# Performance work log

Hardware: AMD Instinct MI355X
Metric: run time of the kernel (lower is better)

## Reference

```python
import jax, jax.numpy as jnp
import numpy as np

D_EMBED = 768
N_HEAD = 12
D_ATTN = D_EMBED // N_HEAD  # 64
SCALE = 1.0 / np.sqrt(D_ATTN)


def setup_inputs() -> dict:
    key = jax.random.key(0)
    ks = jax.random.split(key, 5)
    B, S = 1, 4096
    x = jax.random.normal(ks[0], (B, S, D_EMBED), dtype=jnp.float32)
    # Linear weights stored as [in, out]; init std 0.02 as in _init_weights
    Wq = jax.random.normal(ks[1], (D_EMBED, D_EMBED), dtype=jnp.float32) * 0.02
    Wk = jax.random.normal(ks[2], (D_EMBED, D_EMBED), dtype=jnp.float32) * 0.02
    Wv = jax.random.normal(ks[3], (D_EMBED, D_EMBED), dtype=jnp.float32) * 0.02
    Wo = jax.random.normal(ks[4], (D_EMBED, D_EMBED), dtype=jnp.float32) * 0.02
    gamma = jnp.ones((N_HEAD,), dtype=jnp.float32)
    return {"x": x, "Wq": Wq, "Wk": Wk, "Wv": Wv, "Wo": Wo, "gamma": gamma}


def reference(x, Wq, Wk, Wv, Wo, gamma):
    B, S, _ = x.shape
    # QKV projections (self-attention: k = v = q = x)
    def split_heads(y):
        return y.reshape(B, S, N_HEAD, D_ATTN).transpose(0, 2, 1, 3)  # [B,H,S,D]
    q = split_heads(x @ Wq)
    k = split_heads(x @ Wk)
    v = split_heads(x @ Wv)
    # RBF attention scores: exp(-gamma * scale * ||q - k||^2)
    q_norm = jnp.sum(q * q, axis=-1, keepdims=True)            # [B,H,S,1]
    k_norm = jnp.sum(k * k, axis=-1, keepdims=True)            # [B,H,S,1]
    qk = jnp.einsum('bhsd,bhtd->bhst', q, k)                   # [B,H,S,S]
    dist = jnp.maximum(q_norm - 2.0 * qk + jnp.swapaxes(k_norm, -2, -1), 0.0)
    g = gamma.reshape(1, N_HEAD, 1, 1)
    scores = jnp.exp(-g * SCALE * dist)                        # [B,H,S,S]
    # attn @ V, merge heads, output proj (dropout p=0 -> identity)
    out = jnp.einsum('bhst,bhtd->bhsd', scores, v)
    out = out.transpose(0, 2, 1, 3).reshape(B, S, D_EMBED)
    return out @ Wo
```

## Files before the change

kernel.cpp:

```cpp
#include <hip/hip_runtime.h>
#include <stdint.h>


typedef __attribute__((ext_vector_type(4))) float f32x4;
typedef __attribute__((ext_vector_type(8))) short s16x8;
typedef __attribute__((ext_vector_type(2))) unsigned int u32x2;
typedef __attribute__((ext_vector_type(4))) unsigned int u32x4;

#define S_LEN 4096
#define NHEAD 12
#define DE 768

__device__ __forceinline__ uint16_t f2bf(float f) {
  unsigned u = __float_as_uint(f);
  u += 0x7fffu + ((u >> 16) & 1u);
  return (uint16_t)(u >> 16);
}

__device__ __forceinline__ void gll16(const void* g, void* l) {
  __builtin_amdgcn_global_load_lds(
      (const __attribute__((address_space(1))) unsigned int*)g,
      (__attribute__((address_space(3))) unsigned int*)l, 16, 0, 0);
}

__global__ void k_cvt_x(const float* __restrict__ x, uint16_t* __restrict__ xb) {
  int i = (blockIdx.x * 256 + threadIdx.x) * 4;
  float4 v = *(const float4*)(x + i);
  u32x2 o;
  o.x = (unsigned)f2bf(v.x) | ((unsigned)f2bf(v.y) << 16);
  o.y = (unsigned)f2bf(v.z) | ((unsigned)f2bf(v.w) << 16);
  *(u32x2*)(xb + i) = o;
}

__global__ void k_cvt_w(const float* __restrict__ W0, const float* __restrict__ W1,
                        const float* __restrict__ W2, const float* __restrict__ W3,
                        uint16_t* __restrict__ T0, uint16_t* __restrict__ T1,
                        uint16_t* __restrict__ T2, uint16_t* __restrict__ T3) {
  __shared__ float tile[64][65];
  int z = blockIdx.z;
  const float* W = z == 0 ? W0 : z == 1 ? W1 : z == 2 ? W2 : W3;
  uint16_t* T = z == 0 ? T0 : z == 1 ? T1 : z == 2 ? T2 : T3;
  int r0 = blockIdx.y * 64, c0 = blockIdx.x * 64;
  int t = threadIdx.x;
#pragma unroll
  for (int ii = 0; ii < 16; ++ii) {
    int idx = ii * 256 + t;
    int r = idx >> 6, c = idx & 63;
    tile[r][c] = W[(r0 + r) * DE + c0 + c];
  }
  __syncthreads();
#pragma unroll
  for (int ii = 0; ii < 16; ++ii) {
    int idx = ii * 256 + t;
    int r = idx >> 6, c = idx & 63;
    T[(size_t)(c0 + r) * DE + (r0 + c)] = f2bf(tile[c][r]);
  }
}

template <int MODE>
__global__ __launch_bounds__(256) void k_gemm(
    const uint16_t* __restrict__ A, const uint16_t* __restrict__ B0,
    const uint16_t* __restrict__ B1, const uint16_t* __restrict__ B2,
    uint16_t* __restrict__ Oq, uint16_t* __restrict__ Ok, uint16_t* __restrict__ Ov,
    float* __restrict__ OF) {
  __shared__ __align__(16) uint16_t As[128 * 64];
  __shared__ __align__(16) uint16_t Bs[128 * 64];
  const int K = DE;
  int z = (MODE == 0) ? blockIdx.z : 0;
  const uint16_t* Bt = (MODE == 0) ? (z == 0 ? B0 : z == 1 ? B1 : B2) : B0;
  int m0 = blockIdx.x * 128, n0 = blockIdx.y * 128;
  int tid = threadIdx.x, lane = tid & 63, wid = tid >> 6;
  int G = lane >> 4, c = lane & 15;
  int wr = (wid >> 1) * 64, wc = (wid & 1) * 64;
  f32x4 acc[4][4] = {};
  const char* AsB = (const char*)As;
  const char* BsB = (const char*)Bs;
  for (int kt = 0; kt < K / 64; ++kt) {
#pragma unroll
    for (int i = 0; i < 4; ++i) {
      int L = (i * 256 + tid) * 16;
      int row = L >> 7, ch = (L >> 4) & 7;
      int gch = ch ^ (row & 7);
      gll16((const char*)A + ((size_t)(m0 + row) * K + kt * 64) * 2 + gch * 16,
            (char*)As + i * 4096 + wid * 1024);
      gll16((const char*)Bt + ((size_t)(n0 + row) * K + kt * 64) * 2 + gch * 16,
            (char*)Bs + i * 4096 + wid * 1024);
    }
    __syncthreads();
#pragma unroll
    for (int ks = 0; ks < 2; ++ks) {
      s16x8 a[4], b[4];
#pragma unroll
      for (int mi = 0; mi < 4; ++mi) {
        int row = wr + mi * 16 + c;
        a[mi] = *(const s16x8*)(AsB + row * 128 + (((G + 4 * ks) ^ (row & 7)) << 4));
      }
#pragma unroll
      for (int ni = 0; ni < 4; ++ni) {
        int row = wc + ni * 16 + c;
        b[ni] = *(const s16x8*)(BsB + row * 128 + (((G + 4 * ks) ^ (row & 7)) << 4));
      }
#pragma unroll
      for (int mi = 0; mi < 4; ++mi)
#pragma unroll
        for (int ni = 0; ni < 4; ++ni)
          acc[mi][ni] = __builtin_amdgcn_mfma_f32_16x16x32_bf16(a[mi], b[ni], acc[mi][ni], 0, 0, 0);
    }
    __syncthreads();
  }
#pragma unroll
  for (int mi = 0; mi < 4; ++mi) {
#pragma unroll
    for (int ni = 0; ni < 4; ++ni) {
      int r = m0 + wr + mi * 16 + G * 4;
      int n = n0 + wc + ni * 16 + c;
      if (MODE == 0) {
        int h = n >> 6, d = n & 63;
        if (z < 2) {
          uint16_t* O = (z == 0) ? Oq : Ok;
#pragma unroll
          for (int rr = 0; rr < 4; ++rr)
            O[((size_t)h * S_LEN + (r + rr)) * 64 + d] = f2bf(acc[mi][ni][rr]);
        } else {
          u32x2 pk;
          pk.x = (unsigned)f2bf(acc[mi][ni][0]) | ((unsigned)f2bf(acc[mi][ni][1]) << 16);
          pk.y = (unsigned)f2bf(acc[mi][ni][2]) | ((unsigned)f2bf(acc[mi][ni][3]) << 16);
          *(u32x2*)(Ov + ((size_t)(h * 64 + d)) * S_LEN + r) = pk;
        }
      } else {
#pragma unroll
        for (int rr = 0; rr < 4; ++rr) OF[(size_t)(r + rr) * DE + n] = acc[mi][ni][rr];
      }
    }
  }
}

__global__ void k_norm(const uint16_t* __restrict__ q, const uint16_t* __restrict__ k,
                       float* __restrict__ qn, float* __restrict__ kn) {
  int row = blockIdx.x * 256 + threadIdx.x;
  const int total = NHEAD * S_LEN;
  const uint16_t* src = (row < total) ? q : k;
  float* dst = (row < total) ? qn : kn;
  int r = (row < total) ? row : row - total;
  const u32x4* p = (const u32x4*)(src + (size_t)r * 64);
  float s = 0.f;
#pragma unroll
  for (int i = 0; i < 8; ++i) {
    u32x4 v = p[i];
#pragma unroll
    for (int j = 0; j < 4; ++j) {
      unsigned w = v[j];
      float a = __uint_as_float(w << 16);
      float b = __uint_as_float(w & 0xffff0000u);
      s += a * a + b * b;
    }
  }
  dst[r] = s;
}

__global__ __launch_bounds__(256, 3) void k_attn(
    const uint16_t* __restrict__ q, const uint16_t* __restrict__ k,
    const uint16_t* __restrict__ vT, const float* __restrict__ qn,
    const float* __restrict__ kn, const float* __restrict__ gamma,
    uint16_t* __restrict__ att) {
  __shared__ __align__(16) uint16_t Ks[128 * 64];
  __shared__ __align__(16) uint16_t Vs[64 * 128];
  __shared__ __align__(16) uint16_t Ps[4][16 * 128];
  __shared__ __align__(16) float kns[128];
  int h = blockIdx.y;
  int tid = threadIdx.x, lane = tid & 63, wid = tid >> 6;
  int G = lane >> 4, c = lane & 15;
  int q0 = blockIdx.x * 64 + wid * 16;
  int qg = q0 + c;

  s16x8 qf[2];
  const char* qrow = (const char*)(q + ((size_t)h * S_LEN + qg) * 64);
  qf[0] = *(const s16x8*)(qrow + G * 16);
  qf[1] = *(const s16x8*)(qrow + 64 + G * 16);
  float qn_l = qn[h * S_LEN + qg];
  float coef = -gamma[h] * 0.125f * 1.4426950408889634f;

  f32x4 oacc[4] = {};
  char* PsB = (char*)Ps[wid];
  const char* KsB = (const char*)Ks;
  const char* VsB = (const char*)Vs;
  const char* kbase = (const char*)(k + (size_t)h * S_LEN * 64);
  const char* vbase = (const char*)(vT + (size_t)h * 64 * S_LEN);
  const float* knh = kn + h * S_LEN;

  for (int kt = 0; kt < S_LEN / 128; ++kt) {
#pragma unroll
    for (int i = 0; i < 4; ++i) {
      int L = (i * 256 + tid) * 16;
      int row = L >> 7, ch = (L >> 4) & 7;
      gll16(kbase + (size_t)(kt * 128 + row) * 128 + ((ch ^ (row & 7)) << 4),
            (char*)Ks + i * 4096 + wid * 1024);
    }
#pragma unroll
    for (int i = 0; i < 4; ++i) {
      int L = (i * 256 + tid) * 16;
      int d = L >> 8, ch = (L >> 4) & 15;
      gll16(vbase + (size_t)d * 8192 + kt * 256 + ((ch ^ (d & 15)) << 4),
            (char*)Vs + i * 4096 + wid * 1024);
    }
    if (tid < 32) gll16((const char*)(knh + kt * 128) + tid * 16, (char*)kns);
    __syncthreads();

    f32x4 sacc[8] = {};
#pragma unroll
    for (int fb = 0; fb < 8; ++fb) {
      int kv = fb * 16 + c;
#pragma unroll
      for (int ks = 0; ks < 2; ++ks) {
        s16x8 a = *(const s16x8*)(KsB + kv * 128 + (((G + 4 * ks) ^ (kv & 7)) << 4));
        sacc[fb] = __builtin_amdgcn_mfma_f32_16x16x32_bf16(a, qf[ks], sacc[fb], 0, 0, 0);
      }
    }
#pragma unroll
    for (int fb = 0; fb < 8; ++fb) {
      f32x4 knv = *(const f32x4*)&kns[fb * 16 + G * 4];
      float p0 = __builtin_amdgcn_exp2f(fminf(coef * (qn_l + knv[0] - 2.f * sacc[fb][0]), 0.f));
      float p1 = __builtin_amdgcn_exp2f(fminf(coef * (qn_l + knv[1] - 2.f * sacc[fb][1]), 0.f));
      float p2 = __builtin_amdgcn_exp2f(fminf(coef * (qn_l + knv[2] - 2.f * sacc[fb][2]), 0.f));
      float p3 = __builtin_amdgcn_exp2f(fminf(coef * (qn_l + knv[3] - 2.f * sacc[fb][3]), 0.f));
      u32x2 pw;
      pw.x = (unsigned)f2bf(p0) | ((unsigned)f2bf(p1) << 16);
      pw.y = (unsigned)f2bf(p2) | ((unsigned)f2bf(p3) << 16);
      *(u32x2*)(PsB + c * 256 + ((fb * 32 + 8 * G) ^ ((c & 7) << 4))) = pw;
    }
#pragma unroll
    for (int ks = 0; ks < 4; ++ks) {
      s16x8 bf = *(const s16x8*)(PsB + c * 256 + ((ks * 64 + 16 * G) ^ ((c & 7) << 4)));
#pragma unroll
      for (int fd = 0; fd < 4; ++fd) {
        int d = fd * 16 + c;
        s16x8 a = *(const s16x8*)(VsB + d * 256 + (((G + 4 * ks) ^ (d & 15)) << 4));
        oacc[fd] = __builtin_amdgcn_mfma_f32_16x16x32_bf16(a, bf, oacc[fd], 0, 0, 0);
      }
    }
    __syncthreads();
  }
#pragma unroll
  for (int fd = 0; fd < 4; ++fd) {
    u32x2 pw;
    pw.x = (unsigned)f2bf(oacc[fd][0]) | ((unsigned)f2bf(oacc[fd][1]) << 16);
    pw.y = (unsigned)f2bf(oacc[fd][2]) | ((unsigned)f2bf(oacc[fd][3]) << 16);
    *(u32x2*)(att + (size_t)qg * DE + h * 64 + fd * 16 + G * 4) = pw;
  }
}

extern "C" void kernel_launch(void* const* d_in, const int* in_sizes, int n_in,
                              void* d_out, int out_size, void* d_ws, size_t ws_size,
                              hipStream_t stream) {
  (void)in_sizes; (void)n_in; (void)out_size; (void)ws_size;
  const float* x = (const float*)d_in[0];
  const float* Wq = (const float*)d_in[1];
  const float* Wk = (const float*)d_in[2];
  const float* Wv = (const float*)d_in[3];
  const float* Wo = (const float*)d_in[4];
  const float* gamma = (const float*)d_in[5];

  char* ws = (char*)d_ws;
  uint16_t* xb  = (uint16_t*)(ws);
  uint16_t* wqt = (uint16_t*)(ws + 6291456);
  uint16_t* wkt = (uint16_t*)(ws + 7471104);
  uint16_t* wvt = (uint16_t*)(ws + 8650752);
  uint16_t* wot = (uint16_t*)(ws + 9830400);
  uint16_t* qb  = (uint16_t*)(ws + 11010048);
  uint16_t* kb  = (uint16_t*)(ws + 17301504);
  uint16_t* vTb = (uint16_t*)(ws + 23592960);
  uint16_t* att = (uint16_t*)(ws + 29884416);
  float* qn = (float*)(ws + 36175872);
  float* kn = (float*)(ws + 36372480);

  k_cvt_x<<<3072, 256, 0, stream>>>(x, xb);
  k_cvt_w<<<dim3(12, 12, 4), 256, 0, stream>>>(Wq, Wk, Wv, Wo, wqt, wkt, wvt, wot);
  k_gemm<0><<<dim3(32, 6, 3), 256, 0, stream>>>(xb, wqt, wkt, wvt, qb, kb, vTb, nullptr);
  k_norm<<<384, 256, 0, stream>>>(qb, kb, qn, kn);
  k_attn<<<dim3(64, 12), 256, 0, stream>>>(qb, kb, vTb, qn, kn, gamma, att);
  k_gemm<1><<<dim3(32, 6, 1), 256, 0, stream>>>(att, wot, nullptr, nullptr,
                                                nullptr, nullptr, nullptr, (float*)d_out);
}
```

Before: 153.9 us.

## Factor RBF exponent, split KV across waves, use packed bf16 conversion

The exponent is rewritten as exp2(cq + ck + m2c*qk). The per-query factor exp2(cq) is pulled out of the loop and applied to the output, and the per-key term is pre-scaled by gamma in the norm kernel. This removes the clamp and several FMAs per score. Each wave now handles 32 queries by 64 keys instead of 16 queries by 128 keys, and the two KV halves are reduced through LDS at the end, which raises MFMA reuse of the K and V fragments. It also adds a hardware packed bf16 conversion and s_setprio around the MFMA phases. The risks are that dropping the max(dist,0) clamp and factoring out exp2(cq) can overflow or underflow for large norms, and that the extra accumulators raise register pressure.

```diff
diff --git a/kernel.cpp b/kernel.cpp
--- a/kernel.cpp
+++ b/kernel.cpp
@@ -15,6 +15,12 @@
   unsigned u = __float_as_uint(f);
   u += 0x7fffu + ((u >> 16) & 1u);
   return (uint16_t)(u >> 16);
+}
+
+__device__ __forceinline__ unsigned cvt_pk_bf16(float a, float b) {
+  unsigned r;
+  asm("v_cvt_pk_bf16_f32 %0, %1, %2" : "=v"(r) : "v"(a), "v"(b));
+  return r;
 }
 
 __device__ __forceinline__ void gll16(const void* g, void* l) {
@@ -136,12 +142,14 @@
 }
 
 __global__ void k_norm(const uint16_t* __restrict__ q, const uint16_t* __restrict__ k,
-                       float* __restrict__ qn, float* __restrict__ kn) {
+                       const float* __restrict__ gamma,
+                       float* __restrict__ cqn, float* __restrict__ ckn) {
   int row = blockIdx.x * 256 + threadIdx.x;
   const int total = NHEAD * S_LEN;
   const uint16_t* src = (row < total) ? q : k;
-  float* dst = (row < total) ? qn : kn;
+  float* dst = (row < total) ? cqn : ckn;
   int r = (row < total) ? row : row - total;
+  float coef = -gamma[r >> 12] * 0.18033688011112043f;
   const u32x4* p = (const u32x4*)(src + (size_t)r * 64);
   float s = 0.f;
 #pragma unroll
@@ -155,38 +163,43 @@
       s += a * a + b * b;
     }
   }
-  dst[r] = s;
+  dst[r] = coef * s;
 }
 
 __global__ __launch_bounds__(256, 3) void k_attn(
     const uint16_t* __restrict__ q, const uint16_t* __restrict__ k,
-    const uint16_t* __restrict__ vT, const float* __restrict__ qn,
-    const float* __restrict__ kn, const float* __restrict__ gamma,
+    const uint16_t* __restrict__ vT, const float* __restrict__ cqn,
+    const float* __restrict__ ckn, const float* __restrict__ gamma,
     uint16_t* __restrict__ att) {
   __shared__ __align__(16) uint16_t Ks[128 * 64];
   __shared__ __align__(16) uint16_t Vs[64 * 128];
-  __shared__ __align__(16) uint16_t Ps[4][16 * 128];
-  __shared__ __align__(16) float kns[128];
+  __shared__ __align__(16) uint16_t Ps[4][32 * 64];
+  __shared__ __align__(16) float cks[128];
   int h = blockIdx.y;
   int tid = threadIdx.x, lane = tid & 63, wid = tid >> 6;
   int G = lane >> 4, c = lane & 15;
-  int q0 = blockIdx.x * 64 + wid * 16;
-  int qg = q0 + c;
-
-  s16x8 qf[2];
-  const char* qrow = (const char*)(q + ((size_t)h * S_LEN + qg) * 64);
-  qf[0] = *(const s16x8*)(qrow + G * 16);
-  qf[1] = *(const s16x8*)(qrow + 64 + G * 16);
-  float qn_l = qn[h * S_LEN + qg];
-  float coef = -gamma[h] * 0.125f * 1.4426950408889634f;
-
-  f32x4 oacc[4] = {};
+  int wq = wid & 1, wkv = wid >> 1;
+  int qg0 = blockIdx.x * 64 + wq * 32 + c;
+
+  s16x8 qf[2][2];
+  const char* qb0 = (const char*)(q + ((size_t)h * S_LEN + qg0) * 64);
+#pragma unroll
+  for (int ks = 0; ks < 2; ++ks) {
+    qf[0][ks] = *(const s16x8*)(qb0 + ks * 64 + G * 16);
+    qf[1][ks] = *(const s16x8*)(qb0 + 2048 + ks * 64 + G * 16);
+  }
+  float ebq0 = __builtin_amdgcn_exp2f(cqn[h * S_LEN + qg0]);
+  float ebq1 = __builtin_amdgcn_exp2f(cqn[h * S_LEN + qg0 + 16]);
+  float m2c = gamma[h] * 0.36067376022224085f;
+
+  f32x4 oacc[4][2] = {};
   char* PsB = (char*)Ps[wid];
   const char* KsB = (const char*)Ks;
   const char* VsB = (const char*)Vs;
   const char* kbase = (const char*)(k + (size_t)h * S_LEN * 64);
   const char* vbase = (const char*)(vT + (size_t)h * 64 * S_LEN);
-  const float* knh = kn + h * S_LEN;
+  const float* cknh = ckn + h * S_LEN;
+  int swzP = c & 7;
 
   for (int kt = 0; kt < S_LEN / 128; ++kt) {
 #pragma unroll
@@ -203,49 +216,85 @@
       gll16(vbase + (size_t)d * 8192 + kt * 256 + ((ch ^ (d & 15)) << 4),
             (char*)Vs + i * 4096 + wid * 1024);
     }
-    if (tid < 32) gll16((const char*)(knh + kt * 128) + tid * 16, (char*)kns);
+    if (tid < 32) gll16((const char*)(cknh + kt * 128) + tid * 16, (char*)cks);
     __syncthreads();
 
-    f32x4 sacc[8] = {};
-#pragma unroll
-    for (int fb = 0; fb < 8; ++fb) {
-      int kv = fb * 16 + c;
-#pragma unroll
-      for (int ks = 0; ks < 2; ++ks) {
-        s16x8 a = *(const s16x8*)(KsB + kv * 128 + (((G + 4 * ks) ^ (kv & 7)) << 4));
-        sacc[fb] = __builtin_amdgcn_mfma_f32_16x16x32_bf16(a, qf[ks], sacc[fb], 0, 0, 0);
-      }
-    }
-#pragma unroll
-    for (int fb = 0; fb < 8; ++fb) {
-      f32x4 knv = *(const f32x4*)&kns[fb * 16 + G * 4];
-      float p0 = __builtin_amdgcn_exp2f(fminf(coef * (qn_l + knv[0] - 2.f * sacc[fb][0]), 0.f));
-      float p1 = __builtin_amdgcn_exp2f(fminf(coef * (qn_l + knv[1] - 2.f * sacc[fb][1]), 0.f));
-      float p2 = __builtin_amdgcn_exp2f(fminf(coef * (qn_l + knv[2] - 2.f * sacc[fb][2]), 0.f));
-      float p3 = __builtin_amdgcn_exp2f(fminf(coef * (qn_l + knv[3] - 2.f * sacc[fb][3]), 0.f));
-      u32x2 pw;
-      pw.x = (unsigned)f2bf(p0) | ((unsigned)f2bf(p1) << 16);
-      pw.y = (unsigned)f2bf(p2) | ((unsigned)f2bf(p3) << 16);
-      *(u32x2*)(PsB + c * 256 + ((fb * 32 + 8 * G) ^ ((c & 7) << 4))) = pw;
-    }
-#pragma unroll
-    for (int ks = 0; ks < 4; ++ks) {
-      s16x8 bf = *(const s16x8*)(PsB + c * 256 + ((ks * 64 + 16 * G) ^ ((c & 7) << 4)));
+    f32x4 sacc[4][2] = {};
+    __builtin_amdgcn_s_setprio(1);
+#pragma unroll
+    for (int ks = 0; ks < 2; ++ks) {
+#pragma unroll
+      for (int fb = 0; fb < 4; ++fb) {
+        int row = wkv * 64 + fb * 16 + c;
+        s16x8 a = *(const s16x8*)(KsB + row * 128 + (((G + 4 * ks) ^ (row & 7)) << 4));
+        sacc[fb][0] = __builtin_amdgcn_mfma_f32_16x16x32_bf16(a, qf[0][ks], sacc[fb][0], 0, 0, 0);
+        sacc[fb][1] = __builtin_amdgcn_mfma_f32_16x16x32_bf16(a, qf[1][ks], sacc[fb][1], 0, 0, 0);
+      }
+    }
+    __builtin_amdgcn_s_setprio(0);
+
+#pragma unroll
+    for (int fb = 0; fb < 4; ++fb) {
+      f32x4 ck = *(const f32x4*)&cks[wkv * 64 + fb * 16 + G * 4];
+#pragma unroll
+      for (int qb = 0; qb < 2; ++qb) {
+        f32x4 sv = sacc[fb][qb];
+        float p0 = __builtin_amdgcn_exp2f(ck[0] + m2c * sv[0]);
+        float p1 = __builtin_amdgcn_exp2f(ck[1] + m2c * sv[1]);
+        float p2 = __builtin_amdgcn_exp2f(ck[2] + m2c * sv[2]);
+        float p3 = __builtin_amdgcn_exp2f(ck[3] + m2c * sv[3]);
+        u32x2 pw;
+        pw.x = cvt_pk_bf16(p0, p1);
+        pw.y = cvt_pk_bf16(p2, p3);
+        *(u32x2*)(PsB + (qb * 16 + c) * 128 + (((2 * fb + (G >> 1)) ^ swzP) << 4) + (G & 1) * 8) = pw;
+      }
+    }
+
+    __builtin_amdgcn_s_setprio(1);
+#pragma unroll
+    for (int ks = 0; ks < 2; ++ks) {
+      s16x8 b0 = *(const s16x8*)(PsB + c * 128 + (((G + 4 * ks) ^ swzP) << 4));
+      s16x8 b1 = *(const s16x8*)(PsB + (16 + c) * 128 + (((G + 4 * ks) ^ swzP) << 4));
 #pragma unroll
       for (int fd = 0; fd < 4; ++fd) {
         int d = fd * 16 + c;
-        s16x8 a = *(const s16x8*)(VsB + d * 256 + (((G + 4 * ks) ^ (d & 15)) << 4));
-        oacc[fd] = __builtin_amdgcn_mfma_f32_16x16x32_bf16(a, bf, oacc[fd], 0, 0, 0);
-      }
-    }
+        s16x8 va = *(const s16x8*)(VsB + d * 256 + (((wkv * 8 + G + 4 * ks) ^ (d & 15)) << 4));
+        oacc[fd][0] = __builtin_amdgcn_mfma_f32_16x16x32_bf16(va, b0, oacc[fd][0], 0, 0, 0);
+        oacc[fd][1] = __builtin_amdgcn_mfma_f32_16x16x32_bf16(va, b1, oacc[fd][1], 0, 0, 0);
+      }
+    }
+    __builtin_amdgcn_s_setprio(0);
     __syncthreads();
   }
-#pragma unroll
-  for (int fd = 0; fd < 4; ++fd) {
-    u32x2 pw;
-    pw.x = (unsigned)f2bf(oacc[fd][0]) | ((unsigned)f2bf(oacc[fd][1]) << 16);
-    pw.y = (unsigned)f2bf(oacc[fd][2]) | ((unsigned)f2bf(oacc[fd][3]) << 16);
-    *(u32x2*)(att + (size_t)qg * DE + h * 64 + fd * 16 + G * 4) = pw;
+
+  if (wkv == 1) {
+    float* dst = (float*)Ks + wq * 2048;
+#pragma unroll
+    for (int fd = 0; fd < 4; ++fd)
+#pragma unroll
+      for (int qb = 0; qb < 2; ++qb)
+#pragma unroll
+        for (int r = 0; r < 4; ++r)
+          dst[(fd * 16 + G * 4 + r) * 32 + qb * 16 + c] = oacc[fd][qb][r];
+  }
+  __syncthreads();
+  if (wkv == 0) {
+    const float* srcp = (const float*)Ks + wq * 2048;
+#pragma unroll
+    for (int fd = 0; fd < 4; ++fd) {
+#pragma unroll
+      for (int qb = 0; qb < 2; ++qb) {
+        float eb = qb ? ebq1 : ebq0;
+        f32x4 v;
+#pragma unroll
+        for (int r = 0; r < 4; ++r)
+          v[r] = (oacc[fd][qb][r] + srcp[(fd * 16 + G * 4 + r) * 32 + qb * 16 + c]) * eb;
+        u32x2 w;
+        w.x = cvt_pk_bf16(v[0], v[1]);
+        w.y = cvt_pk_bf16(v[2], v[3]);
+        *(u32x2*)(att + (size_t)(qg0 + qb * 16) * DE + h * 64 + fd * 16 + G * 4) = w;
+      }
+    }
   }
 }
 
@@ -270,14 +319,14 @@
   uint16_t* kb  = (uint16_t*)(ws + 17301504);
   uint16_t* vTb = (uint16_t*)(ws + 23592960);
   uint16_t* att = (uint16_t*)(ws + 29884416);
-  float* qn = (float*)(ws + 36175872);
-  float* kn = (float*)(ws + 36372480);
+  float* cqn = (float*)(ws + 36175872);
+  float* ckn = (float*)(ws + 36372480);
 
   k_cvt_x<<<3072, 256, 0, stream>>>(x, xb);
   k_cvt_w<<<dim3(12, 12, 4), 256, 0, stream>>>(Wq, Wk, Wv, Wo, wqt, wkt, wvt, wot);
   k_gemm<0><<<dim3(32, 6, 3), 256, 0, stream>>>(xb, wqt, wkt, wvt, qb, kb, vTb, nullptr);
-  k_norm<<<384, 256, 0, stream>>>(qb, kb, qn, kn);
-  k_attn<<<dim3(64, 12), 256, 0, stream>>>(qb, kb, vTb, qn, kn, gamma, att);
+  k_norm<<<384, 256, 0, stream>>>(qb, kb, gamma, cqn, ckn);
+  k_attn<<<dim3(64, 12), 256, 0, stream>>>(qb, kb, vTb, cqn, ckn, gamma, att);
   k_gemm<1><<<dim3(32, 6, 1), 256, 0, stream>>>(att, wot, nullptr, nullptr,
                                                 nullptr, nullptr, nullptr, (float*)d_out);
 }
```

New measurement: 130.8 us. 15.0% less time.
